# Optimization experiments

Measured on AMD Instinct MI355X. Metric: run time of the kernel, lower is better.

Reference implementation:

```python
import jax, jax.numpy as jnp
import numpy as np

THRESHOLD = 0.5


def setup_inputs() -> dict:
    key = jax.random.key(0)
    k1, k2, k3, k4 = jax.random.split(key, 4)
    N, HW, A, C = 32, 4096, 5, 80
    return {
        "box": jax.random.normal(k1, (N, HW, A, 4), dtype=jnp.float32),
        "box_confidence": jax.random.uniform(k2, (N, HW, A, 1), dtype=jnp.float32),
        "class_score": jax.random.uniform(k3, (N, HW, A, C), dtype=jnp.float32),
        "prior": jax.random.uniform(k4, (HW, A, 4), dtype=jnp.float32),
        "feat_size": 64,
    }


def reference(box, box_confidence, class_score, prior, feat_size):
    # 1) add prior offsets to centers, scale width/height by prior size
    xy = box[..., :2] + prior[..., :2]          # (N, HW, A, 2)
    wh = box[..., 2:] * prior[..., 2:]          # (N, HW, A, 2)
    # 2) center format -> corner format, normalize to [0,1] by feat_size
    half = wh * 0.5
    corners = jnp.concatenate([xy - half, xy + half], axis=-1) / feat_size  # (N, HW, A, 4)
    # 3) choose_box: per-box class score = objectness * class prob; threshold filter.
    #    (Data-dependent compaction is expressed as masking for jit-compatibility.)
    scores = box_confidence * class_score       # (N, HW, A, C)
    class_probs = jnp.max(scores, axis=-1)      # (N, HW, A)
    class_index = jnp.argmax(scores, axis=-1).astype(jnp.int32)  # (N, HW, A)
    mask = class_probs > THRESHOLD
    box_out = jnp.where(mask[..., None], corners, 0.0)
    probs_out = jnp.where(mask, class_probs, 0.0)
    return box_out, probs_out, class_index
```

## Files before the change

### kernel.cpp

```cpp
#include <hip/hip_runtime.h>

#define NBOX (32 * 4096 * 5)
#define HWA  (4096 * 5)
#define NCLS 80
#define THRESHOLD 0.5f

__global__ __launch_bounds__(256) void detector_kernel(
    const float4* __restrict__ box,
    const float*  __restrict__ conf,
    const float*  __restrict__ cls,
    const float4* __restrict__ prior,
    const unsigned int* __restrict__ fs_word,
    float4* __restrict__ box_out,
    float*  __restrict__ probs_out,
    float*  __restrict__ idx_out)
{
    const int tid = blockIdx.x * blockDim.x + threadIdx.x;
    if (tid >= NBOX) return;

    const unsigned int w = *fs_word;
    const float fs  = (w < 1000000u) ? (float)w : __uint_as_float(w);
    const float inv = 1.0f / fs;

    const float4 b = box[tid];
    const float4 p = prior[tid % HWA];
    const float cx = b.x + p.x;
    const float cy = b.y + p.y;
    const float hx = (b.z * p.z) * 0.5f;
    const float hy = (b.w * p.w) * 0.5f;
    float4 corner;
    corner.x = (cx - hx) * inv;
    corner.y = (cy - hy) * inv;
    corner.z = (cx + hx) * inv;
    corner.w = (cy + hy) * inv;

    const float cf = conf[tid];
    const float4* cv = (const float4*)(cls + (size_t)tid * NCLS);
    float m = -INFINITY;
    int   mi = 0;
#pragma unroll
    for (int j = 0; j < NCLS / 4; ++j) {
        const float4 v = cv[j];
        const float s0 = cf * v.x;
        const float s1 = cf * v.y;
        const float s2 = cf * v.z;
        const float s3 = cf * v.w;
        if (s0 > m) { m = s0; mi = 4 * j;     }
        if (s1 > m) { m = s1; mi = 4 * j + 1; }
        if (s2 > m) { m = s2; mi = 4 * j + 2; }
        if (s3 > m) { m = s3; mi = 4 * j + 3; }
    }

    const bool keep = (m > THRESHOLD);
    float4 bo;
    bo.x = keep ? corner.x : 0.0f;
    bo.y = keep ? corner.y : 0.0f;
    bo.z = keep ? corner.z : 0.0f;
    bo.w = keep ? corner.w : 0.0f;

    box_out[tid]   = bo;
    probs_out[tid] = keep ? m : 0.0f;
    idx_out[tid]   = (float)mi;
}

extern "C" void kernel_launch(void* const* d_in, const int* in_sizes, int n_in,
                              void* d_out, int out_size, void* d_ws, size_t ws_size,
                              hipStream_t stream) {
    const float4* box   = (const float4*)d_in[0];
    const float*  conf  = (const float*)d_in[1];
    const float*  cls   = (const float*)d_in[2];
    const float4* prior = (const float4*)d_in[3];
    const unsigned int* fs = (const unsigned int*)d_in[4];

    float* out = (float*)d_out;
    float4* box_out  = (float4*)out;
    float* probs_out = out + (size_t)4 * NBOX;
    float* idx_out   = probs_out + NBOX;

    const int threads = 256;
    const int blocks  = (NBOX + threads - 1) / threads;
    detector_kernel<<<blocks, threads, 0, stream>>>(
        box, conf, cls, prior, fs, box_out, probs_out, idx_out);
}
```

Baseline: 317.8 us.

## Split each box's class scan across four lanes with shuffle reduction

Each box's 80-class argmax is now split across four lanes. Each lane loads five float4 values at interleaved offsets so that neighbouring lanes read contiguous memory, and the partial maxima are combined with xor shuffles on a packed (score, inverted index) key that keeps the first-occurrence tie-break. This replaces the old strided per-thread reads of 320-byte rows, which coalesced poorly. The cost is four times as many threads, extra shuffles, and only 16 of 64 lanes doing the box math and stores, so the write phase runs at quarter occupancy per wave.

```diff
diff --git a/kernel.cpp b/kernel.cpp
--- a/kernel.cpp
+++ b/kernel.cpp
@@ -2,65 +2,81 @@
 
 #define NBOX (32 * 4096 * 5)
 #define HWA  (4096 * 5)
-#define NCLS 80
 #define THRESHOLD 0.5f
 
 __global__ __launch_bounds__(256) void detector_kernel(
     const float4* __restrict__ box,
     const float*  __restrict__ conf,
-    const float*  __restrict__ cls,
+    const float4* __restrict__ cls4,
     const float4* __restrict__ prior,
     const unsigned int* __restrict__ fs_word,
     float4* __restrict__ box_out,
     float*  __restrict__ probs_out,
     float*  __restrict__ idx_out)
 {
-    const int tid = blockIdx.x * blockDim.x + threadIdx.x;
-    if (tid >= NBOX) return;
+    const int t       = threadIdx.x;
+    const int lane    = t & 63;
+    const int waveIdx = blockIdx.x * 4 + (t >> 6);
+    const int boxBase = waveIdx * 16;
+    const int slot    = lane & 3;
+    const int myBox   = boxBase + (lane >> 2);
 
+    const int obox = boxBase + (lane & 15);
+    const float4 b = box[obox];
+    const float4 p = prior[obox % HWA];
     const unsigned int w = *fs_word;
+
+    const float cf = conf[myBox];
+
+    const float4* row = cls4 + (size_t)myBox * 20 + slot;
+    const float4 v0 = row[0];
+    const float4 v1 = row[4];
+    const float4 v2 = row[8];
+    const float4 v3 = row[12];
+    const float4 v4 = row[16];
+
+    float m  = -1.0f;
+    int   mi = 0;
+    const int c0 = slot * 4;
+#define STEP(V, K) { \
+        const float s0 = cf * (V).x, s1 = cf * (V).y, s2 = cf * (V).z, s3 = cf * (V).w; \
+        const int c = c0 + 16 * (K); \
+        if (s0 > m) { m = s0; mi = c;     } \
+        if (s1 > m) { m = s1; mi = c + 1; } \
+        if (s2 > m) { m = s2; mi = c + 2; } \
+        if (s3 > m) { m = s3; mi = c + 3; } }
+    STEP(v0, 0) STEP(v1, 1) STEP(v2, 2) STEP(v3, 3) STEP(v4, 4)
+#undef STEP
+
+    unsigned long long packed =
+        ((unsigned long long)__float_as_uint(m) << 32) | (unsigned int)(127 - mi);
+    unsigned long long o;
+    o = __shfl_xor(packed, 1, 64); if (o > packed) packed = o;
+    o = __shfl_xor(packed, 2, 64); if (o > packed) packed = o;
+
+    const unsigned long long res = __shfl(packed, (lane & 15) * 4, 64);
+
     const float fs  = (w < 1000000u) ? (float)w : __uint_as_float(w);
     const float inv = 1.0f / fs;
-
-    const float4 b = box[tid];
-    const float4 p = prior[tid % HWA];
     const float cx = b.x + p.x;
     const float cy = b.y + p.y;
     const float hx = (b.z * p.z) * 0.5f;
     const float hy = (b.w * p.w) * 0.5f;
-    float4 corner;
-    corner.x = (cx - hx) * inv;
-    corner.y = (cy - hy) * inv;
-    corner.z = (cx + hx) * inv;
-    corner.w = (cy + hy) * inv;
 
-    const float cf = conf[tid];
-    const float4* cv = (const float4*)(cls + (size_t)tid * NCLS);
-    float m = -INFINITY;
-    int   mi = 0;
-#pragma unroll
-    for (int j = 0; j < NCLS / 4; ++j) {
-        const float4 v = cv[j];
-        const float s0 = cf * v.x;
-        const float s1 = cf * v.y;
-        const float s2 = cf * v.z;
-        const float s3 = cf * v.w;
-        if (s0 > m) { m = s0; mi = 4 * j;     }
-        if (s1 > m) { m = s1; mi = 4 * j + 1; }
-        if (s2 > m) { m = s2; mi = 4 * j + 2; }
-        if (s3 > m) { m = s3; mi = 4 * j + 3; }
+    const float mm   = __uint_as_float((unsigned int)(res >> 32));
+    const int   midx = 127 - (int)(res & 0x7Fu);
+    const bool  keep = (mm > THRESHOLD);
+
+    if (lane < 16) {
+        float4 bo;
+        bo.x = keep ? (cx - hx) * inv : 0.0f;
+        bo.y = keep ? (cy - hy) * inv : 0.0f;
+        bo.z = keep ? (cx + hx) * inv : 0.0f;
+        bo.w = keep ? (cy + hy) * inv : 0.0f;
+        box_out[obox]   = bo;
+        probs_out[obox] = keep ? mm : 0.0f;
+        idx_out[obox]   = (float)midx;
     }
-
-    const bool keep = (m > THRESHOLD);
-    float4 bo;
-    bo.x = keep ? corner.x : 0.0f;
-    bo.y = keep ? corner.y : 0.0f;
-    bo.z = keep ? corner.z : 0.0f;
-    bo.w = keep ? corner.w : 0.0f;
-
-    box_out[tid]   = bo;
-    probs_out[tid] = keep ? m : 0.0f;
-    idx_out[tid]   = (float)mi;
 }
 
 extern "C" void kernel_launch(void* const* d_in, const int* in_sizes, int n_in,
@@ -68,7 +84,7 @@
                               hipStream_t stream) {
     const float4* box   = (const float4*)d_in[0];
     const float*  conf  = (const float*)d_in[1];
-    const float*  cls   = (const float*)d_in[2];
+    const float4* cls4  = (const float4*)d_in[2];
     const float4* prior = (const float4*)d_in[3];
     const unsigned int* fs = (const unsigned int*)d_in[4];
 
@@ -77,8 +93,7 @@
     float* probs_out = out + (size_t)4 * NBOX;
     float* idx_out   = probs_out + NBOX;
 
-    const int threads = 256;
-    const int blocks  = (NBOX + threads - 1) / threads;
-    detector_kernel<<<blocks, threads, 0, stream>>>(
-        box, conf, cls, prior, fs, box_out, probs_out, idx_out);
+    const int blocks = NBOX / 64;
+    detector_kernel<<<blocks, 256, 0, stream>>>(
+        box, conf, cls4, prior, fs, box_out, probs_out, idx_out);
 }
```

New measurement: 302.6 us. 4.8% less time.
